# Performance work log

Hardware: AMD Instinct MI355X
Metric: run time of the kernel (lower is better)

## Reference

```python
import jax, jax.numpy as jnp
import numpy as np

B, N, D_POINTS, D_MODEL = 2, 65536, 64, 128
SCALE = 1.0 / np.float32(np.sqrt(D_MODEL))


def setup_inputs() -> dict:
    key = jax.random.key(0)
    ks = jax.random.split(key, 20)
    def lin(k, fan_in, fan_out):
        s = 1.0 / np.sqrt(fan_in)
        return jax.random.uniform(k, (fan_in, fan_out), jnp.float32, -s, s)
    return {
        "xyz": jax.random.normal(ks[0], (B, N, 3), jnp.float32),
        "features": jax.random.normal(ks[1], (B, N, D_POINTS), jnp.float32),
        "fc1_w": lin(ks[2], D_POINTS, D_MODEL), "fc1_b": jnp.zeros((D_MODEL,), jnp.float32),
        "fc2_w": lin(ks[3], D_MODEL, D_POINTS), "fc2_b": jnp.zeros((D_POINTS,), jnp.float32),
        "d1_w": lin(ks[4], 3, D_MODEL), "d1_b": jnp.zeros((D_MODEL,), jnp.float32),
        "d2_w": lin(ks[5], D_MODEL, D_MODEL), "d2_b": jnp.zeros((D_MODEL,), jnp.float32),
        "g1_w": lin(ks[6], D_MODEL, D_MODEL), "g1_b": jnp.zeros((D_MODEL,), jnp.float32),
        "g2_w": lin(ks[7], D_MODEL, D_MODEL), "g2_b": jnp.zeros((D_MODEL,), jnp.float32),
        "wq": lin(ks[8], D_MODEL, D_MODEL),
        "wk": lin(ks[9], D_MODEL, D_MODEL),
        "wv": lin(ks[10], D_MODEL, D_MODEL),
    }


def reference(xyz, features, fc1_w, fc1_b, fc2_w, fc2_b, d1_w, d1_b, d2_w, d2_b,
              g1_w, g1_b, g2_w, g2_b, wq, wk, wv):
    # x: [B, N, d_model]
    x = features @ fc1_w + fc1_b
    q = x @ wq
    k = x @ wk
    v = x @ wv
    # position encoding MLP on xyz: [B, N, d_model]
    pos_enc = jax.nn.relu(xyz @ d1_w + d1_b) @ d2_w + d2_b
    # vector attention: elementwise q - k + pos_enc, gamma MLP, per-channel softmax over points
    attn = jax.nn.relu((q - k + pos_enc) @ g1_w + g1_b) @ g2_w + g2_b
    attn = jax.nn.softmax(attn * SCALE, axis=-2)  # softmax over N (point axis)
    # elementwise gating of values
    res = attn * (v + pos_enc)
    res = res @ fc2_w + fc2_b + features  # residual
    return (res, attn)
```

## Files before the change

kernel.cpp:

```cpp
#include <hip/hip_runtime.h>
#include <hip/hip_bf16.h>

#define BB 2
#define NN 65536
#define DP 64
#define DM 128
#define SCALEF 0.08838834764831845f

typedef __attribute__((ext_vector_type(8))) short short8v;
typedef __attribute__((ext_vector_type(4))) float float4v;

__device__ __forceinline__ unsigned short f2bf(float f) {
  unsigned u = __float_as_uint(f);
  u += 0x7FFFu + ((u >> 16) & 1u);
  return (unsigned short)(u >> 16);
}
__device__ __forceinline__ float bf2f(unsigned short h) {
  return __uint_as_float(((unsigned)h) << 16);
}

__global__ __launch_bounds__(256) void k0_kernel(
    const float* __restrict__ wq, const float* __restrict__ wk,
    const float* __restrict__ fc1_w, const float* __restrict__ fc2_w,
    const float* __restrict__ d2_w, const float* __restrict__ g1_w,
    const float* __restrict__ g2_w, const float* __restrict__ wv_w,
    float* __restrict__ sums,
    short* __restrict__ d2t, short* __restrict__ fc1t, short* __restrict__ wqkt,
    short* __restrict__ g1t, short* __restrict__ g2t, short* __restrict__ wvt,
    short* __restrict__ fc2t) {
  int t = threadIdx.x, bi = blockIdx.x;
  if (bi == 0) sums[t] = 0.f;
  int mat = bi >> 5, blk = bi & 31;
  if (mat == 1) {
    int i = blk * 256 + t;
    int n = i >> 6, k = i & 63;
    fc1t[n * 64 + k] = (short)f2bf(fc1_w[k * 128 + n]);
  } else if (mat == 6) {
    int i = blk * 256 + t;
    int n = i >> 7, k = i & 127;
    fc2t[n * 128 + k] = (short)f2bf(fc2_w[k * 64 + n]);
  } else {
    const float* src = (mat == 0) ? d2_w : (mat == 2) ? wq : (mat == 3) ? g1_w
                     : (mat == 4) ? g2_w : wv_w;
    short* dst = (mat == 0) ? d2t : (mat == 2) ? wqkt : (mat == 3) ? g1t
               : (mat == 4) ? g2t : wvt;
#pragma unroll
    for (int j = 0; j < 2; ++j) {
      int i = blk * 512 + t + j * 256;
      int n = i >> 7, k = i & 127;
      float v = src[k * 128 + n];
      if (mat == 2) v -= wk[k * 128 + n];
      dst[n * 128 + k] = (short)f2bf(v);
    }
  }
}

template<int K>
__device__ __forceinline__ void loadB(const short* __restrict__ Wt,
                                      int wid, int col, int quad, short8v b[2][4]) {
#pragma unroll
  for (int nt = 0; nt < 2; ++nt)
#pragma unroll
    for (int kt = 0; kt < K / 32; ++kt)
      b[nt][kt] = *(const short8v*)(Wt + (wid * 32 + nt * 16 + col) * K + kt * 32 + quad * 8);
}

template<int K>
__device__ __forceinline__ void gemm_compute(const short* __restrict__ A,
                                             const short8v b[2][4],
                                             int col, int quad, float4v acc[4][2]) {
#pragma unroll
  for (int kt = 0; kt < K / 32; ++kt) {
#pragma unroll
    for (int mt = 0; mt < 4; ++mt) {
      short8v a = *(const short8v*)(A + (mt * 16 + col) * 136 + kt * 32 + quad * 8);
      acc[mt][0] = __builtin_amdgcn_mfma_f32_16x16x32_bf16(a, b[0][kt], acc[mt][0], 0, 0, 0);
      acc[mt][1] = __builtin_amdgcn_mfma_f32_16x16x32_bf16(a, b[1][kt], acc[mt][1], 0, 0, 0);
    }
  }
}

__device__ __forceinline__ void store_tile(short* __restrict__ dst,
                                           const float4v acc[4][2],
                                           int wid, int col, int quad,
                                           float b0, float b1, bool do_relu) {
#pragma unroll
  for (int mt = 0; mt < 4; ++mt)
#pragma unroll
    for (int nt = 0; nt < 2; ++nt) {
      float bias = nt ? b1 : b0;
#pragma unroll
      for (int r = 0; r < 4; ++r) {
        float v = acc[mt][nt][r] + bias;
        if (do_relu) v = fmaxf(v, 0.f);
        dst[(mt * 16 + quad * 4 + r) * 136 + wid * 32 + nt * 16 + col] = (short)f2bf(v);
      }
    }
}

#define ZERO_ACC(acc) \
  _Pragma("unroll") for (int mt = 0; mt < 4; ++mt) \
  _Pragma("unroll") for (int nt = 0; nt < 2; ++nt) \
  _Pragma("unroll") for (int r = 0; r < 4; ++r) acc[mt][nt][r] = 0.f;

__global__ __launch_bounds__(256, 3) void k1_kernel(
    const float* __restrict__ xyz, const float* __restrict__ features,
    const short* __restrict__ fc1t, const float* __restrict__ fc1_b,
    const float* __restrict__ d1_w, const float* __restrict__ d1_b,
    const short* __restrict__ d2t, const float* __restrict__ d2_b,
    const short* __restrict__ g1t, const float* __restrict__ g1_b,
    const short* __restrict__ g2t, const float* __restrict__ g2_b,
    const short* __restrict__ wqkt, const short* __restrict__ wvt,
    unsigned short* __restrict__ Ebf, unsigned short* __restrict__ Gbf,
    float* __restrict__ sums) {
  __shared__ __align__(16) short As[64 * 136];
  __shared__ __align__(16) short Xs[64 * 136];

  const int tid = threadIdx.x;
  const int wid = tid >> 6, lane = tid & 63;
  const int col = lane & 15, quad = lane >> 4;
  const long long p0 = (long long)blockIdx.x * 64;
  const int bi = (int)(p0 >> 16);

  short8v b[2][4];
  loadB<128>(d2t, wid, col, quad, b);

  float* xf = (float*)Xs;
  if (tid < 192) xf[tid] = xyz[p0 * 3 + tid];
  __syncthreads();

  {
    const int tn = tid & 31, tm = tid >> 5;
    const int c4 = tn * 4, pbase = tm * 8;
    float4 w0 = *(const float4*)(d1_w + c4);
    float4 w1 = *(const float4*)(d1_w + 128 + c4);
    float4 w2 = *(const float4*)(d1_w + 256 + c4);
    float4 bb = *(const float4*)(d1_b + c4);
#pragma unroll
    for (int p = 0; p < 8; ++p) {
      float x0 = xf[(pbase + p) * 3 + 0];
      float x1 = xf[(pbase + p) * 3 + 1];
      float x2 = xf[(pbase + p) * 3 + 2];
      short4 rr;
      rr.x = (short)f2bf(fmaxf(0.f, fmaf(x0, w0.x, fmaf(x1, w1.x, fmaf(x2, w2.x, bb.x)))));
      rr.y = (short)f2bf(fmaxf(0.f, fmaf(x0, w0.y, fmaf(x1, w1.y, fmaf(x2, w2.y, bb.y)))));
      rr.z = (short)f2bf(fmaxf(0.f, fmaf(x0, w0.z, fmaf(x1, w1.z, fmaf(x2, w2.z, bb.z)))));
      rr.w = (short)f2bf(fmaxf(0.f, fmaf(x0, w0.w, fmaf(x1, w1.w, fmaf(x2, w2.w, bb.w)))));
      *(short4*)(As + (pbase + p) * 136 + c4) = rr;
    }
  }
  __syncthreads();

  const int ch0 = wid * 32 + col, ch1 = ch0 + 16;
  float4v pe[4][2], acc[4][2];

  ZERO_ACC(acc)
  gemm_compute<128>(As, b, col, quad, acc);
  {
    float b0 = d2_b[ch0], b1 = d2_b[ch1];
#pragma unroll
    for (int mt = 0; mt < 4; ++mt)
#pragma unroll
      for (int r = 0; r < 4; ++r) {
        pe[mt][0][r] = acc[mt][0][r] + b0;
        pe[mt][1][r] = acc[mt][1][r] + b1;
      }
  }
  loadB<64>(fc1t, wid, col, quad, b);
  __syncthreads();

#pragma unroll
  for (int j = 0; j < 4; ++j) {
    int c = tid + j * 256;
    float4 f = *(const float4*)(features + p0 * 64 + (long long)c * 4);
    int row = c >> 4, cp = (c & 15) * 4;
    short4 s;
    s.x = (short)f2bf(f.x); s.y = (short)f2bf(f.y);
    s.z = (short)f2bf(f.z); s.w = (short)f2bf(f.w);
    *(short4*)(As + row * 136 + cp) = s;
  }
  __syncthreads();

  ZERO_ACC(acc)
  gemm_compute<64>(As, b, col, quad, acc);
  store_tile(Xs, acc, wid, col, quad, fc1_b[ch0], fc1_b[ch1], false);
  loadB<128>(wqkt, wid, col, quad, b);
  __syncthreads();

#pragma unroll
  for (int mt = 0; mt < 4; ++mt)
#pragma unroll
    for (int nt = 0; nt < 2; ++nt)
#pragma unroll
      for (int r = 0; r < 4; ++r) acc[mt][nt][r] = pe[mt][nt][r];
  gemm_compute<128>(Xs, b, col, quad, acc);
  store_tile(As, acc, wid, col, quad, 0.f, 0.f, false);
  loadB<128>(g1t, wid, col, quad, b);
  __syncthreads();

  ZERO_ACC(acc)
  gemm_compute<128>(As, b, col, quad, acc);
  __syncthreads();
  store_tile(As, acc, wid, col, quad, g1_b[ch0], g1_b[ch1], true);
  loadB<128>(g2t, wid, col, quad, b);
  __syncthreads();

  ZERO_ACC(acc)
  gemm_compute<128>(As, b, col, quad, acc);
  {
    float b0 = g2_b[ch0], b1 = g2_b[ch1];
    float s0 = 0.f, s1 = 0.f;
#pragma unroll
    for (int mt = 0; mt < 4; ++mt)
#pragma unroll
      for (int r = 0; r < 4; ++r) {
        long long row = p0 + mt * 16 + quad * 4 + r;
        float e0 = __expf((acc[mt][0][r] + b0) * SCALEF);
        float e1 = __expf((acc[mt][1][r] + b1) * SCALEF);
        Ebf[row * DM + ch0] = f2bf(e0);
        Ebf[row * DM + ch1] = f2bf(e1);
        s0 += e0; s1 += e1;
      }
    s0 += __shfl_xor(s0, 16, 64); s0 += __shfl_xor(s0, 32, 64);
    s1 += __shfl_xor(s1, 16, 64); s1 += __shfl_xor(s1, 32, 64);
    if (quad == 0) {
      atomicAdd(&sums[bi * DM + ch0], s0);
      atomicAdd(&sums[bi * DM + ch1], s1);
    }
  }

  loadB<128>(wvt, wid, col, quad, b);
#pragma unroll
  for (int mt = 0; mt < 4; ++mt)
#pragma unroll
    for (int nt = 0; nt < 2; ++nt)
#pragma unroll
      for (int r = 0; r < 4; ++r) acc[mt][nt][r] = pe[mt][nt][r];
  gemm_compute<128>(Xs, b, col, quad, acc);
#pragma unroll
  for (int mt = 0; mt < 4; ++mt)
#pragma unroll
    for (int r = 0; r < 4; ++r) {
      long long row = p0 + mt * 16 + quad * 4 + r;
      Gbf[row * DM + ch0] = f2bf(acc[mt][0][r]);
      Gbf[row * DM + ch1] = f2bf(acc[mt][1][r]);
    }
}

__global__ __launch_bounds__(256) void k3_kernel(
    const unsigned short* __restrict__ Ebf, float* __restrict__ out_attn,
    float* __restrict__ out_res, const unsigned short* __restrict__ Gbf,
    const float* __restrict__ sums,
    const short* __restrict__ fc2t, const float* __restrict__ fc2_b,
    const float* __restrict__ features) {
  __shared__ __align__(16) short Ys[64 * 136];
  const int tid = threadIdx.x;
  const long long p0 = (long long)blockIdx.x * 64;
  const int bi = (int)(p0 >> 16);

  {
    const int tn = tid & 31, tm = tid >> 5;
    const int c4 = tn * 4;
    float4 sv = *(const float4*)(sums + bi * DM + c4);
    float4 rs;
    rs.x = 1.f / sv.x; rs.y = 1.f / sv.y; rs.z = 1.f / sv.z; rs.w = 1.f / sv.w;
#pragma unroll
    for (int pr = 0; pr < 8; ++pr) {
      int p = tm * 8 + pr;
      long long idx = (p0 + p) * DM + c4;
      ushort4 e = *(const ushort4*)(Ebf + idx);
      float4 a;
      a.x = bf2f(e.x) * rs.x; a.y = bf2f(e.y) * rs.y;
      a.z = bf2f(e.z) * rs.z; a.w = bf2f(e.w) * rs.w;
      *(float4*)(out_attn + idx) = a;
      ushort4 g = *(const ushort4*)(Gbf + idx);
      short4 y;
      y.x = (short)f2bf(a.x * bf2f(g.x)); y.y = (short)f2bf(a.y * bf2f(g.y));
      y.z = (short)f2bf(a.z * bf2f(g.z)); y.w = (short)f2bf(a.w * bf2f(g.w));
      *(short4*)(Ys + p * 136 + c4) = y;
    }
  }

  const int wid = tid >> 6, lane = tid & 63;
  const int col = lane & 15, quad = lane >> 4;
  const int n = wid * 16 + col;
  short8v bw[4];
#pragma unroll
  for (int kt = 0; kt < 4; ++kt)
    bw[kt] = *(const short8v*)(fc2t + n * DM + kt * 32 + quad * 8);
  __syncthreads();

  float4v acc[4];
#pragma unroll
  for (int mt = 0; mt < 4; ++mt)
#pragma unroll
    for (int r = 0; r < 4; ++r) acc[mt][r] = 0.f;
#pragma unroll
  for (int kt = 0; kt < 4; ++kt)
#pragma unroll
    for (int mt = 0; mt < 4; ++mt) {
      short8v a = *(const short8v*)(Ys + (mt * 16 + col) * 136 + kt * 32 + quad * 8);
      acc[mt] = __builtin_amdgcn_mfma_f32_16x16x32_bf16(a, bw[kt], acc[mt], 0, 0, 0);
    }
  float bb = fc2_b[n];
#pragma unroll
  for (int mt = 0; mt < 4; ++mt)
#pragma unroll
    for (int r = 0; r < 4; ++r) {
      long long row = p0 + mt * 16 + quad * 4 + r;
      out_res[row * DP + n] = acc[mt][r] + bb + features[row * DP + n];
    }
}

extern "C" void kernel_launch(void* const* d_in, const int* in_sizes, int n_in,
                              void* d_out, int out_size, void* d_ws, size_t ws_size,
                              hipStream_t stream) {
  const float* xyz      = (const float*)d_in[0];
  const float* features = (const float*)d_in[1];
  const float* fc1_w    = (const float*)d_in[2];
  const float* fc1_b    = (const float*)d_in[3];
  const float* fc2_w    = (const float*)d_in[4];
  const float* fc2_b    = (const float*)d_in[5];
  const float* d1_w     = (const float*)d_in[6];
  const float* d1_b     = (const float*)d_in[7];
  const float* d2_w     = (const float*)d_in[8];
  const float* d2_b     = (const float*)d_in[9];
  const float* g1_w     = (const float*)d_in[10];
  const float* g1_b     = (const float*)d_in[11];
  const float* g2_w     = (const float*)d_in[12];
  const float* g2_b     = (const float*)d_in[13];
  const float* wq       = (const float*)d_in[14];
  const float* wk       = (const float*)d_in[15];
  const float* wv       = (const float*)d_in[16];

  float* out_res  = (float*)d_out;
  float* out_attn = out_res + (long long)BB * NN * DP;

  float* sums = (float*)d_ws;
  short* d2t  = (short*)(sums + 256);
  short* fc1t = d2t + 16384;
  short* wqkt = fc1t + 8192;
  short* g1t  = wqkt + 16384;
  short* g2t  = g1t + 16384;
  short* wvt  = g2t + 16384;
  short* fc2t = wvt + 16384;
  unsigned short* Ebf = (unsigned short*)(fc2t + 8192);
  unsigned short* Gbf = (unsigned short*)d_out;

  hipLaunchKernelGGL(k0_kernel, dim3(224), dim3(256), 0, stream,
                     wq, wk, fc1_w, fc2_w, d2_w, g1_w, g2_w, wv,
                     sums, d2t, fc1t, wqkt, g1t, g2t, wvt, fc2t);
  hipLaunchKernelGGL(k1_kernel, dim3((BB * NN) / 64), dim3(256), 0, stream,
                     xyz, features, fc1t, fc1_b, d1_w, d1_b, d2t, d2_b,
                     g1t, g1_b, g2t, g2_b, wqkt, wvt, Ebf, Gbf, sums);
  hipLaunchKernelGGL(k3_kernel, dim3((BB * NN) / 64), dim3(256), 0, stream,
                     Ebf, out_attn, out_res, Gbf, sums, fc2t, fc2_b, features);
}
```

Before: 237.1 us.

## Halve point tile to 32 rows, raise occupancy, vectorize k3 loads/stores

```diff
diff --git a/kernel.cpp b/kernel.cpp
--- a/kernel.cpp
+++ b/kernel.cpp
@@ -68,11 +68,11 @@
 template<int K>
 __device__ __forceinline__ void gemm_compute(const short* __restrict__ A,
                                              const short8v b[2][4],
-                                             int col, int quad, float4v acc[4][2]) {
+                                             int col, int quad, float4v acc[2][2]) {
 #pragma unroll
   for (int kt = 0; kt < K / 32; ++kt) {
 #pragma unroll
-    for (int mt = 0; mt < 4; ++mt) {
+    for (int mt = 0; mt < 2; ++mt) {
       short8v a = *(const short8v*)(A + (mt * 16 + col) * 136 + kt * 32 + quad * 8);
       acc[mt][0] = __builtin_amdgcn_mfma_f32_16x16x32_bf16(a, b[0][kt], acc[mt][0], 0, 0, 0);
       acc[mt][1] = __builtin_amdgcn_mfma_f32_16x16x32_bf16(a, b[1][kt], acc[mt][1], 0, 0, 0);
@@ -81,11 +81,11 @@
 }
 
 __device__ __forceinline__ void store_tile(short* __restrict__ dst,
-                                           const float4v acc[4][2],
+                                           const float4v acc[2][2],
                                            int wid, int col, int quad,
                                            float b0, float b1, bool do_relu) {
 #pragma unroll
-  for (int mt = 0; mt < 4; ++mt)
+  for (int mt = 0; mt < 2; ++mt)
 #pragma unroll
     for (int nt = 0; nt < 2; ++nt) {
       float bias = nt ? b1 : b0;
@@ -99,11 +99,11 @@
 }
 
 #define ZERO_ACC(acc) \
-  _Pragma("unroll") for (int mt = 0; mt < 4; ++mt) \
+  _Pragma("unroll") for (int mt = 0; mt < 2; ++mt) \
   _Pragma("unroll") for (int nt = 0; nt < 2; ++nt) \
   _Pragma("unroll") for (int r = 0; r < 4; ++r) acc[mt][nt][r] = 0.f;
 
-__global__ __launch_bounds__(256, 3) void k1_kernel(
+__global__ __launch_bounds__(256, 5) void k1_kernel(
     const float* __restrict__ xyz, const float* __restrict__ features,
     const short* __restrict__ fc1t, const float* __restrict__ fc1_b,
     const float* __restrict__ d1_w, const float* __restrict__ d1_b,
@@ -113,31 +113,31 @@
     const short* __restrict__ wqkt, const short* __restrict__ wvt,
     unsigned short* __restrict__ Ebf, unsigned short* __restrict__ Gbf,
     float* __restrict__ sums) {
-  __shared__ __align__(16) short As[64 * 136];
-  __shared__ __align__(16) short Xs[64 * 136];
+  __shared__ __align__(16) short As[32 * 136];
+  __shared__ __align__(16) short Xs[32 * 136];
 
   const int tid = threadIdx.x;
   const int wid = tid >> 6, lane = tid & 63;
   const int col = lane & 15, quad = lane >> 4;
-  const long long p0 = (long long)blockIdx.x * 64;
+  const long long p0 = (long long)blockIdx.x * 32;
   const int bi = (int)(p0 >> 16);
 
   short8v b[2][4];
   loadB<128>(d2t, wid, col, quad, b);
 
   float* xf = (float*)Xs;
-  if (tid < 192) xf[tid] = xyz[p0 * 3 + tid];
+  if (tid < 96) xf[tid] = xyz[p0 * 3 + tid];
   __syncthreads();
 
   {
     const int tn = tid & 31, tm = tid >> 5;
-    const int c4 = tn * 4, pbase = tm * 8;
+    const int c4 = tn * 4, pbase = tm * 4;
     float4 w0 = *(const float4*)(d1_w + c4);
     float4 w1 = *(const float4*)(d1_w + 128 + c4);
     float4 w2 = *(const float4*)(d1_w + 256 + c4);
     float4 bb = *(const float4*)(d1_b + c4);
 #pragma unroll
-    for (int p = 0; p < 8; ++p) {
+    for (int p = 0; p < 4; ++p) {
       float x0 = xf[(pbase + p) * 3 + 0];
       float x1 = xf[(pbase + p) * 3 + 1];
       float x2 = xf[(pbase + p) * 3 + 2];
@@ -152,14 +152,14 @@
   __syncthreads();
 
   const int ch0 = wid * 32 + col, ch1 = ch0 + 16;
-  float4v pe[4][2], acc[4][2];
+  float4v pe[2][2], acc[2][2];
 
   ZERO_ACC(acc)
   gemm_compute<128>(As, b, col, quad, acc);
   {
     float b0 = d2_b[ch0], b1 = d2_b[ch1];
 #pragma unroll
-    for (int mt = 0; mt < 4; ++mt)
+    for (int mt = 0; mt < 2; ++mt)
 #pragma unroll
       for (int r = 0; r < 4; ++r) {
         pe[mt][0][r] = acc[mt][0][r] + b0;
@@ -170,7 +170,7 @@
   __syncthreads();
 
 #pragma unroll
-  for (int j = 0; j < 4; ++j) {
+  for (int j = 0; j < 2; ++j) {
     int c = tid + j * 256;
     float4 f = *(const float4*)(features + p0 * 64 + (long long)c * 4);
     int row = c >> 4, cp = (c & 15) * 4;
@@ -188,7 +188,7 @@
   __syncthreads();
 
 #pragma unroll
-  for (int mt = 0; mt < 4; ++mt)
+  for (int mt = 0; mt < 2; ++mt)
 #pragma unroll
     for (int nt = 0; nt < 2; ++nt)
 #pragma unroll
@@ -208,10 +208,12 @@
   ZERO_ACC(acc)
   gemm_compute<128>(As, b, col, quad, acc);
   {
+    short8v b2[2][4];
+    loadB<128>(wvt, wid, col, quad, b2);
     float b0 = g2_b[ch0], b1 = g2_b[ch1];
     float s0 = 0.f, s1 = 0.f;
 #pragma unroll
-    for (int mt = 0; mt < 4; ++mt)
+    for (int mt = 0; mt < 2; ++mt)
 #pragma unroll
       for (int r = 0; r < 4; ++r) {
         long long row = p0 + mt * 16 + quad * 4 + r;
@@ -227,57 +229,64 @@
       atomicAdd(&sums[bi * DM + ch0], s0);
       atomicAdd(&sums[bi * DM + ch1], s1);
     }
-  }
-
-  loadB<128>(wvt, wid, col, quad, b);
-#pragma unroll
-  for (int mt = 0; mt < 4; ++mt)
-#pragma unroll
-    for (int nt = 0; nt < 2; ++nt)
-#pragma unroll
-      for (int r = 0; r < 4; ++r) acc[mt][nt][r] = pe[mt][nt][r];
-  gemm_compute<128>(Xs, b, col, quad, acc);
-#pragma unroll
-  for (int mt = 0; mt < 4; ++mt)
-#pragma unroll
-    for (int r = 0; r < 4; ++r) {
-      long long row = p0 + mt * 16 + quad * 4 + r;
-      Gbf[row * DM + ch0] = f2bf(acc[mt][0][r]);
-      Gbf[row * DM + ch1] = f2bf(acc[mt][1][r]);
-    }
-}
-
-__global__ __launch_bounds__(256) void k3_kernel(
+
+#pragma unroll
+    for (int mt = 0; mt < 2; ++mt)
+#pragma unroll
+      for (int nt = 0; nt < 2; ++nt)
+#pragma unroll
+        for (int r = 0; r < 4; ++r) acc[mt][nt][r] = pe[mt][nt][r];
+    gemm_compute<128>(Xs, b2, col, quad, acc);
+#pragma unroll
+    for (int mt = 0; mt < 2; ++mt)
+#pragma unroll
+      for (int r = 0; r < 4; ++r) {
+        long long row = p0 + mt * 16 + quad * 4 + r;
+        Gbf[row * DM + ch0] = f2bf(acc[mt][0][r]);
+        Gbf[row * DM + ch1] = f2bf(acc[mt][1][r]);
+      }
+  }
+}
+
+__global__ __launch_bounds__(256, 5) void k3_kernel(
     const unsigned short* __restrict__ Ebf, float* __restrict__ out_attn,
     float* __restrict__ out_res, const unsigned short* __restrict__ Gbf,
     const float* __restrict__ sums,
     const short* __restrict__ fc2t, const float* __restrict__ fc2_b,
     const float* __restrict__ features) {
-  __shared__ __align__(16) short Ys[64 * 136];
+  __shared__ __align__(16) short Ys[32 * 136];
   const int tid = threadIdx.x;
-  const long long p0 = (long long)blockIdx.x * 64;
+  const long long p0 = (long long)blockIdx.x * 32;
   const int bi = (int)(p0 >> 16);
 
   {
-    const int tn = tid & 31, tm = tid >> 5;
-    const int c4 = tn * 4;
-    float4 sv = *(const float4*)(sums + bi * DM + c4);
-    float4 rs;
-    rs.x = 1.f / sv.x; rs.y = 1.f / sv.y; rs.z = 1.f / sv.z; rs.w = 1.f / sv.w;
-#pragma unroll
-    for (int pr = 0; pr < 8; ++pr) {
-      int p = tm * 8 + pr;
-      long long idx = (p0 + p) * DM + c4;
-      ushort4 e = *(const ushort4*)(Ebf + idx);
-      float4 a;
-      a.x = bf2f(e.x) * rs.x; a.y = bf2f(e.y) * rs.y;
-      a.z = bf2f(e.z) * rs.z; a.w = bf2f(e.w) * rs.w;
-      *(float4*)(out_attn + idx) = a;
-      ushort4 g = *(const ushort4*)(Gbf + idx);
-      short4 y;
-      y.x = (short)f2bf(a.x * bf2f(g.x)); y.y = (short)f2bf(a.y * bf2f(g.y));
-      y.z = (short)f2bf(a.z * bf2f(g.z)); y.w = (short)f2bf(a.w * bf2f(g.w));
-      *(short4*)(Ys + p * 136 + c4) = y;
+    const int tn = tid & 15, tm = tid >> 4;
+    const int c8 = tn * 8;
+    float4 sv0 = *(const float4*)(sums + bi * DM + c8);
+    float4 sv1 = *(const float4*)(sums + bi * DM + c8 + 4);
+    float4 r0, r1;
+    r0.x = 1.f / sv0.x; r0.y = 1.f / sv0.y; r0.z = 1.f / sv0.z; r0.w = 1.f / sv0.w;
+    r1.x = 1.f / sv1.x; r1.y = 1.f / sv1.y; r1.z = 1.f / sv1.z; r1.w = 1.f / sv1.w;
+#pragma unroll
+    for (int it = 0; it < 2; ++it) {
+      int row = tm + it * 16;
+      long long idx = (p0 + row) * DM + c8;
+      short8v e8 = *(const short8v*)(Ebf + idx);
+      short8v g8 = *(const short8v*)(Gbf + idx);
+      float a[8];
+      a[0] = bf2f((unsigned short)e8[0]) * r0.x; a[1] = bf2f((unsigned short)e8[1]) * r0.y;
+      a[2] = bf2f((unsigned short)e8[2]) * r0.z; a[3] = bf2f((unsigned short)e8[3]) * r0.w;
+      a[4] = bf2f((unsigned short)e8[4]) * r1.x; a[5] = bf2f((unsigned short)e8[5]) * r1.y;
+      a[6] = bf2f((unsigned short)e8[6]) * r1.z; a[7] = bf2f((unsigned short)e8[7]) * r1.w;
+      float4 a0 = {a[0], a[1], a[2], a[3]};
+      float4 a1 = {a[4], a[5], a[6], a[7]};
+      *(float4*)(out_attn + idx) = a0;
+      *(float4*)(out_attn + idx + 4) = a1;
+      short8v y;
+#pragma unroll
+      for (int q = 0; q < 8; ++q)
+        y[q] = (short)f2bf(a[q] * bf2f((unsigned short)g8[q]));
+      *(short8v*)(Ys + row * 136 + c8) = y;
     }
   }
 
@@ -290,26 +299,38 @@
     bw[kt] = *(const short8v*)(fc2t + n * DM + kt * 32 + quad * 8);
   __syncthreads();
 
-  float4v acc[4];
-#pragma unroll
-  for (int mt = 0; mt < 4; ++mt)
+  float4v acc[2];
+#pragma unroll
+  for (int mt = 0; mt < 2; ++mt)
 #pragma unroll
     for (int r = 0; r < 4; ++r) acc[mt][r] = 0.f;
 #pragma unroll
   for (int kt = 0; kt < 4; ++kt)
 #pragma unroll
-    for (int mt = 0; mt < 4; ++mt) {
+    for (int mt = 0; mt < 2; ++mt) {
       short8v a = *(const short8v*)(Ys + (mt * 16 + col) * 136 + kt * 32 + quad * 8);
       acc[mt] = __builtin_amdgcn_mfma_f32_16x16x32_bf16(a, bw[kt], acc[mt], 0, 0, 0);
     }
+  __syncthreads();
+  float* yf = (float*)Ys;
   float bb = fc2_b[n];
 #pragma unroll
-  for (int mt = 0; mt < 4; ++mt)
-#pragma unroll
-    for (int r = 0; r < 4; ++r) {
-      long long row = p0 + mt * 16 + quad * 4 + r;
-      out_res[row * DP + n] = acc[mt][r] + bb + features[row * DP + n];
-    }
+  for (int mt = 0; mt < 2; ++mt)
+#pragma unroll
+    for (int r = 0; r < 4; ++r)
+      yf[(mt * 16 + quad * 4 + r) * 68 + n] = acc[mt][r] + bb;
+  __syncthreads();
+
+#pragma unroll
+  for (int it = 0; it < 2; ++it) {
+    int idx = tid + it * 256;
+    int row = idx >> 4, ch = idx & 15;
+    float4 v = *(const float4*)(yf + row * 68 + ch * 4);
+    float4 ft = *(const float4*)(features + (p0 + row) * DP + ch * 4);
+    float4 o;
+    o.x = v.x + ft.x; o.y = v.y + ft.y; o.z = v.z + ft.z; o.w = v.w + ft.w;
+    *(float4*)(out_res + (p0 + row) * DP + ch * 4) = o;
+  }
 }
 
 extern "C" void kernel_launch(void* const* d_in, const int* in_sizes, int n_in,
@@ -350,9 +371,9 @@
   hipLaunchKernelGGL(k0_kernel, dim3(224), dim3(256), 0, stream,
                      wq, wk, fc1_w, fc2_w, d2_w, g1_w, g2_w, wv,
                      sums, d2t, fc1t, wqkt, g1t, g2t, wvt, fc2t);
-  hipLaunchKernelGGL(k1_kernel, dim3((BB * NN) / 64), dim3(256), 0, stream,
+  hipLaunchKernelGGL(k1_kernel, dim3((BB * NN) / 32), dim3(256), 0, stream,
                      xyz, features, fc1t, fc1_b, d1_w, d1_b, d2t, d2_b,
                      g1t, g1_b, g2t, g2_b, wqkt, wvt, Ebf, Gbf, sums);
-  hipLaunchKernelGGL(k3_kernel, dim3((BB * NN) / 64), dim3(256), 0, stream,
+  hipLaunchKernelGGL(k3_kernel, dim3((BB * NN) / 32), dim3(256), 0, stream,
                      Ebf, out_attn, out_res, Gbf, sums, fc2t, fc2_b, features);
 }
```

Measured after the change: 283.9 us. +19.7%, slower.
